# Kernel tuning notes

Measured on AMD Instinct MI355X. Metric: run time of the kernel, lower is better.

The kernel has to match this reference:

```python
import jax, jax.numpy as jnp
import numpy as np

BLOCK = 16  # NVFP4 block size (per-block FP8 scale over 16 FP4 values)
FP4_GRID = jnp.array([0.0, 0.5, 1.0, 1.5, 2.0, 3.0, 4.0, 6.0], dtype=jnp.float32)
FP4_MIDS = jnp.array([0.25, 0.75, 1.25, 1.75, 2.5, 3.5, 5.0], dtype=jnp.float32)


def _quantize_fp4(v):
    # round-to-nearest onto the signed E2M1 grid {0,.5,1,1.5,2,3,4,6}
    a = jnp.clip(jnp.abs(v), 0.0, 6.0)
    idx = jnp.searchsorted(FP4_MIDS, a)
    return jnp.sign(v) * FP4_GRID[idx]


def _block_quantize(x):
    # returns (fp4 values, per-16-block scales) such that x ~= q * scale_blocked
    M, K = x.shape
    B = K // BLOCK
    xb = x.reshape(M, B, BLOCK)
    s = jnp.max(jnp.abs(xb), axis=-1) / 6.0 + 1e-8  # [M, B]
    q = _quantize_fp4(xb / s[:, :, None]).reshape(M, K)
    return q, s


def setup_inputs() -> dict:
    key = jax.random.key(0)
    k1, k2, k3 = jax.random.split(key, 3)
    M, K, N = 8192, 4096, 4096
    bsz, q_len = 4, 2048

    x_raw = jax.random.normal(k1, (M, K), dtype=jnp.float32)
    w_raw = jax.random.normal(k2, (N, K), dtype=jnp.float32) * 0.02

    # global weight scale as in NVFP4_reorder_quantize_w: max(w)/(448*6)
    scale_w_global = jnp.max(w_raw) / (448.0 * 6.0)
    qw, scale_w = _block_quantize(w_raw / scale_w_global)

    # activation global scale (produced upstream by the activation quantizer)
    scale_x_global = jnp.max(x_raw) / (448.0 * 6.0)
    qx, scale_x = _block_quantize(x_raw / scale_x_global)

    bias = jax.random.normal(k3, (N,), dtype=jnp.float32) * 0.01

    return {
        "qx": qx,                      # [M, K] FP4-grid values
        "scale_x": scale_x,            # [M, K//16] block scales
        "scale": scale_x_global,       # scalar global activation scale
        "qw": qw,                      # [N, K] FP4-grid values
        "scale_w": scale_w,            # [N, K//16] block scales
        "scale_w_global": scale_w_global,
        "bias": bias,                  # [N]
        "bsz": bsz,
        "q_len": q_len,
    }


def reference(qx, scale_x, scale, qw, scale_w, scale_w_global, bias, bsz, q_len):
    # Dequant-scaled GEMM: y = (qx .* sx)(qw .* sw)^T * (scale * scale_w_global) + bias
    M, K = qx.shape
    N = qw.shape[0]
    B = K // BLOCK
    xd = (qx.reshape(M, B, BLOCK) * scale_x[:, :, None]).reshape(M, K)
    wd = (qw.reshape(N, B, BLOCK) * scale_w[:, :, None]).reshape(N, K)
    y = jnp.einsum("mk,nk->mn", xd, wd) * (scale * scale_w_global)
    y = y + bias
    return y.reshape(bsz, q_len, -1)
```

## Files before the change

### kernel.cpp

```cpp
#include <hip/hip_runtime.h>
#include <cstdint>

#define K_DIM 4096
#define ROWB 13
#define NU   (K_DIM / 32)

typedef __bf16 bf16x8 __attribute__((ext_vector_type(8)));
typedef float f32x4 __attribute__((ext_vector_type(4)));

__device__ inline unsigned short f2bf(float f) {
    union { float f; unsigned int u; } v; v.f = f;
    unsigned int u = v.u;
    return (unsigned short)((u + 0x7FFFu + ((u >> 16) & 1u)) >> 16);
}

__device__ __forceinline__ void gload16(const void* g, void* l) {
    __builtin_amdgcn_global_load_lds(
        (const __attribute__((address_space(1))) unsigned int*)g,
        (__attribute__((address_space(3))) unsigned int*)l,
        16, 0, 0);
}

__global__ __launch_bounds__(256) void dequant2_kernel(
        const float* __restrict__ qx, const float* __restrict__ sx,
        unsigned short* __restrict__ xd, long t8x,
        const float* __restrict__ qw, const float* __restrict__ sw,
        unsigned short* __restrict__ wd, long t8w) {
    long i = (long)blockIdx.x * blockDim.x + threadIdx.x;
    if (i >= t8x + t8w) return;
    const float* q; const float* s; unsigned short* o;
    if (i < t8x) { q = qx; s = sx; o = xd; }
    else         { q = qw; s = sw; o = wd; i -= t8x; }
    long e = i * 8;
    float sc = s[e >> 4];
    float4 v0 = *(const float4*)(q + e);
    float4 v1 = *(const float4*)(q + e + 4);
    union { unsigned short h[8]; uint4 u; } ov;
    ov.h[0] = f2bf(v0.x * sc); ov.h[1] = f2bf(v0.y * sc);
    ov.h[2] = f2bf(v0.z * sc); ov.h[3] = f2bf(v0.w * sc);
    ov.h[4] = f2bf(v1.x * sc); ov.h[5] = f2bf(v1.y * sc);
    ov.h[6] = f2bf(v1.z * sc); ov.h[7] = f2bf(v1.w * sc);
    *(uint4*)(o + e) = ov.u;
}


__global__ __launch_bounds__(256, 2) void gemm128x256_kernel(
        const unsigned short* __restrict__ A,
        const unsigned short* __restrict__ B,
        const float* __restrict__ sg1, const float* __restrict__ sg2,
        const float* __restrict__ bias,
        float* __restrict__ out, int M, int N) {
    __shared__ __align__(16) char lds[73728];

    const int tid  = threadIdx.x;
    const int lane = tid & 63;
    const int wid  = tid >> 6;
    const int l15  = lane & 15;
    const int cb   = (lane >> 4) << 4;
    const int scb  = ((lane & 3) ^ ((lane >> 3) & 3)) << 4;

    const int nbn = N >> 8;
    const int nwg = (M >> 7) * nbn;
    const int cpx = nwg >> 3;
    const int bid = blockIdx.x;
    const int swz = (bid & 7) * cpx + (bid >> 3);
    const int tile_m = (swz / nbn) << 7;
    const int tile_n = (swz % nbn) << 8;

    const int grow = lane >> 2;
    const char* gA0 = (const char*)A +
        ((size_t)(tile_m + 32 * wid + grow) << ROWB) + scb;
    const char* gB0 = (const char*)B +
        ((size_t)(tile_n + 64 * wid + grow) << ROWB) + scb;
    const int dA0 = wid * 2048;
    const int dB0 = 8192 + wid * 4096;

    const int aoff = l15 * 64 + (cb ^ (((l15 >> 1) & 3) << 4));
    const int brow = wid * 64 + l15;
    const int boff = 8192 + brow * 64 + (cb ^ (((brow >> 1) & 3) << 4));

    f32x4 acc[8][4];
#pragma unroll
    for (int mb = 0; mb < 8; ++mb)
#pragma unroll
        for (int nb = 0; nb < 4; ++nb) acc[mb][nb] = (f32x4){0.f, 0.f, 0.f, 0.f};

#pragma unroll
    for (int pu = 0; pu < 2; ++pu) {
        char* Sb = lds + pu * 24576;
        const int kb = pu << 6;
        gload16(gA0 + kb, Sb + dA0);
        gload16(gA0 + kb + ((size_t)16 << ROWB), Sb + dA0 + 1024);
        gload16(gB0 + kb, Sb + dB0);
        gload16(gB0 + kb + ((size_t)16 << ROWB), Sb + dB0 + 1024);
        gload16(gB0 + kb + ((size_t)32 << ROWB), Sb + dB0 + 2048);
        gload16(gB0 + kb + ((size_t)48 << ROWB), Sb + dB0 + 3072);
    }
    asm volatile("s_waitcnt vmcnt(6)" ::: "memory");
    __builtin_amdgcn_s_barrier();

#define UNIT_BODY(SKU, CUR, STG) do {                                        \
    const int skb = (SKU) << 6;                                              \
    bf16x8 bfr[4], afr[4], afr2[4];                                          \
    _Pragma("unroll")                                                        \
    for (int nb = 0; nb < 4; ++nb)                                           \
        bfr[nb] = *(const bf16x8*)(lds + (CUR) + boff + nb * 1024);          \
    _Pragma("unroll")                                                        \
    for (int mb = 0; mb < 4; ++mb)                                           \
        afr[mb] = *(const bf16x8*)(lds + (CUR) + aoff + mb * 1024);          \
    gload16(gA0 + skb, lds + (STG) + dA0);                                   \
    gload16(gA0 + skb + ((size_t)16 << ROWB), lds + (STG) + dA0 + 1024);     \
    gload16(gB0 + skb, lds + (STG) + dB0);                                   \
    __builtin_amdgcn_s_barrier();                                            \
    __builtin_amdgcn_s_setprio(1);                                           \
    _Pragma("unroll")                                                        \
    for (int mb = 0; mb < 4; ++mb)                                           \
        _Pragma("unroll")                                                    \
        for (int nb = 0; nb < 4; ++nb)                                       \
            acc[mb][nb] = __builtin_amdgcn_mfma_f32_16x16x32_bf16(           \
                afr[mb], bfr[nb], acc[mb][nb], 0, 0, 0);                     \
    __builtin_amdgcn_s_setprio(0);                                           \
    _Pragma("unroll")                                                        \
    for (int mb = 0; mb < 4; ++mb)                                           \
        afr2[mb] = *(const bf16x8*)(lds + (CUR) + aoff + 4096 + mb * 1024);  \
    gload16(gB0 + skb + ((size_t)16 << ROWB), lds + (STG) + dB0 + 1024);     \
    gload16(gB0 + skb + ((size_t)32 << ROWB), lds + (STG) + dB0 + 2048);     \
    gload16(gB0 + skb + ((size_t)48 << ROWB), lds + (STG) + dB0 + 3072);     \
    __builtin_amdgcn_s_barrier();                                            \
    __builtin_amdgcn_s_setprio(1);                                           \
    _Pragma("unroll")                                                        \
    for (int mb = 0; mb < 4; ++mb)                                           \
        _Pragma("unroll")                                                    \
        for (int nb = 0; nb < 4; ++nb)                                       \
            acc[mb + 4][nb] = __builtin_amdgcn_mfma_f32_16x16x32_bf16(       \
                afr2[mb], bfr[nb], acc[mb + 4][nb], 0, 0, 0);                \
    __builtin_amdgcn_s_setprio(0);                                           \
    asm volatile("s_waitcnt vmcnt(6)" ::: "memory");                         \
    __builtin_amdgcn_s_barrier();                                            \
} while (0)

    for (int ub = 0; ub < 126; ub += 3) {
        UNIT_BODY(ub + 2, 0,     49152);
        UNIT_BODY(ub + 3, 24576, 0);
        UNIT_BODY(ub + 4, 49152, 24576);
    }
    UNIT_BODY(127, 0,     49152);
    UNIT_BODY(127, 24576, 0);
#undef UNIT_BODY

    const float gs = sg1[0] * sg2[0];
    const int row0 = tile_m + ((lane >> 4) << 2);
    const int col0 = tile_n + wid * 64 + l15;
    float bv[4];
#pragma unroll
    for (int nb = 0; nb < 4; ++nb) bv[nb] = bias[col0 + nb * 16];
#pragma unroll
    for (int mb = 0; mb < 8; ++mb)
#pragma unroll
        for (int nb = 0; nb < 4; ++nb) {
            const int col = col0 + nb * 16;
#pragma unroll
            for (int j = 0; j < 4; ++j)
                out[(size_t)(row0 + mb * 16 + j) * N + col] =
                    acc[mb][nb][j] * gs + bv[nb];
        }
}

__global__ __launch_bounds__(256) void gemm_fused_kernel(
        const float* __restrict__ qx, const float* __restrict__ sx,
        const float* __restrict__ qw, const float* __restrict__ sw,
        const float* __restrict__ sg1, const float* __restrict__ sg2,
        const float* __restrict__ bias,
        float* __restrict__ out, int M, int N) {
    __shared__ __align__(16) unsigned short As[128 * 32];
    __shared__ __align__(16) unsigned short Bs[128 * 32];
    const int tid  = threadIdx.x;
    const int lane = tid & 63;
    const int wid  = tid >> 6;
    const int tile_n = blockIdx.x * 128;
    const int tile_m = blockIdx.y * 128;
    const int wm = wid >> 1, wn = wid & 1;
    f32x4 acc[16];
#pragma unroll
    for (int i = 0; i < 16; ++i) acc[i] = (f32x4){0.f, 0.f, 0.f, 0.f};
    const int l15 = lane & 15;
    const int lk  = (lane >> 4) * 8;
    for (int kt = 0; kt < K_DIM / 32; ++kt) {
#pragma unroll
        for (int cc = 0; cc < 2; ++cc) {
            const int c   = tid + cc * 256;
            const int row = c >> 2;
            const int col = (c & 3) * 8;
            const int gk  = kt * 32 + col;
            {
                const float* qp = qx + (long)(tile_m + row) * K_DIM + gk;
                float s = sx[(long)(tile_m + row) * (K_DIM / 16) + (gk >> 4)];
                float4 a0 = *(const float4*)qp;
                float4 a1 = *(const float4*)(qp + 4);
                union { unsigned short h[8]; uint4 u; } o;
                o.h[0] = f2bf(a0.x * s); o.h[1] = f2bf(a0.y * s);
                o.h[2] = f2bf(a0.z * s); o.h[3] = f2bf(a0.w * s);
                o.h[4] = f2bf(a1.x * s); o.h[5] = f2bf(a1.y * s);
                o.h[6] = f2bf(a1.z * s); o.h[7] = f2bf(a1.w * s);
                *(uint4*)&As[row * 32 + col] = o.u;
            }
            {
                const float* qp = qw + (long)(tile_n + row) * K_DIM + gk;
                float s = sw[(long)(tile_n + row) * (K_DIM / 16) + (gk >> 4)];
                float4 a0 = *(const float4*)qp;
                float4 a1 = *(const float4*)(qp + 4);
                union { unsigned short h[8]; uint4 u; } o;
                o.h[0] = f2bf(a0.x * s); o.h[1] = f2bf(a0.y * s);
                o.h[2] = f2bf(a0.z * s); o.h[3] = f2bf(a0.w * s);
                o.h[4] = f2bf(a1.x * s); o.h[5] = f2bf(a1.y * s);
                o.h[6] = f2bf(a1.z * s); o.h[7] = f2bf(a1.w * s);
                *(uint4*)&Bs[row * 32 + col] = o.u;
            }
        }
        __syncthreads();
        const unsigned short* pa = As + (wm * 64 + l15) * 32 + lk;
        const unsigned short* pb = Bs + (wn * 64 + l15) * 32 + lk;
        bf16x8 a[4], b[4];
#pragma unroll
        for (int i = 0; i < 4; ++i) {
            a[i] = *(const bf16x8*)(pa + i * 16 * 32);
            b[i] = *(const bf16x8*)(pb + i * 16 * 32);
        }
#pragma unroll
        for (int mi = 0; mi < 4; ++mi)
#pragma unroll
            for (int ni = 0; ni < 4; ++ni)
                acc[mi * 4 + ni] = __builtin_amdgcn_mfma_f32_16x16x32_bf16(
                    a[mi], b[ni], acc[mi * 4 + ni], 0, 0, 0);
        __syncthreads();
    }
    const float gs = sg1[0] * sg2[0];
    const int row0 = tile_m + wm * 64 + (lane >> 4) * 4;
    const int col0 = tile_n + wn * 64 + l15;
#pragma unroll
    for (int mi = 0; mi < 4; ++mi)
#pragma unroll
        for (int ni = 0; ni < 4; ++ni) {
            const int col = col0 + ni * 16;
            const float bv = bias[col];
#pragma unroll
            for (int j = 0; j < 4; ++j)
                out[(long)(row0 + mi * 16 + j) * N + col] =
                    acc[mi * 4 + ni][j] * gs + bv;
        }
}

extern "C" void kernel_launch(void* const* d_in, const int* in_sizes, int n_in,
                              void* d_out, int out_size, void* d_ws, size_t ws_size,
                              hipStream_t stream) {
    const float* qx   = (const float*)d_in[0];
    const float* sx   = (const float*)d_in[1];
    const float* sc   = (const float*)d_in[2];
    const float* qw   = (const float*)d_in[3];
    const float* sw   = (const float*)d_in[4];
    const float* swg  = (const float*)d_in[5];
    const float* bias = (const float*)d_in[6];
    float* out = (float*)d_out;

    const int M = in_sizes[0] / K_DIM;
    const int N = in_sizes[3] / K_DIM;

    const size_t needA = (size_t)M * K_DIM * sizeof(unsigned short);
    const size_t needB = (size_t)N * K_DIM * sizeof(unsigned short);

    if (ws_size >= needA + needB) {
        unsigned short* xd = (unsigned short*)d_ws;
        unsigned short* wd = (unsigned short*)((char*)d_ws + needA);
        long t8x = (long)M * K_DIM / 8;
        long t8w = (long)N * K_DIM / 8;
        long tot = t8x + t8w;
        dequant2_kernel<<<(int)((tot + 255) / 256), 256, 0, stream>>>(
            qx, sx, xd, t8x, qw, sw, wd, t8w);
        const int nwg = (M / 128) * (N / 256);
        gemm128x256_kernel<<<nwg, 256, 0, stream>>>(xd, wd, sc, swg, bias, out, M, N);
    } else {
        dim3 grid(N / 128, M / 128);
        gemm_fused_kernel<<<grid, 256, 0, stream>>>(
            qx, sx, qw, sw, sc, swg, bias, out, M, N);
    }
}
```

Baseline: 323.3 us.

## Use 256x256 tiles with 8 waves, streaming B fragments from global into registers

```diff
diff --git a/kernel.cpp b/kernel.cpp
--- a/kernel.cpp
+++ b/kernel.cpp
@@ -44,40 +44,42 @@
 }
 
 
-__global__ __launch_bounds__(256, 2) void gemm128x256_kernel(
+__global__ __launch_bounds__(512, 2) void gemm256_kernel(
         const unsigned short* __restrict__ A,
         const unsigned short* __restrict__ B,
         const float* __restrict__ sg1, const float* __restrict__ sg2,
         const float* __restrict__ bias,
         float* __restrict__ out, int M, int N) {
-    __shared__ __align__(16) char lds[73728];
+    __shared__ __align__(16) char lds[65536];
 
     const int tid  = threadIdx.x;
     const int lane = tid & 63;
     const int wid  = tid >> 6;
+    const int wm   = wid >> 2;
+    const int wn   = wid & 3;
     const int l15  = lane & 15;
     const int cb   = (lane >> 4) << 4;
     const int scb  = ((lane & 3) ^ ((lane >> 3) & 3)) << 4;
 
-    const int nbn = N >> 8;
-    const int nwg = (M >> 7) * nbn;
+    const int nbm = M >> 8;
+    const int nwg = nbm * (N >> 8);
     const int cpx = nwg >> 3;
     const int bid = blockIdx.x;
     const int swz = (bid & 7) * cpx + (bid >> 3);
-    const int tile_m = (swz / nbn) << 7;
-    const int tile_n = (swz % nbn) << 8;
+    const int tile_n = (swz / nbm) << 8;
+    const int tile_m = (swz % nbm) << 8;
 
     const int grow = lane >> 2;
     const char* gA0 = (const char*)A +
         ((size_t)(tile_m + 32 * wid + grow) << ROWB) + scb;
-    const char* gB0 = (const char*)B +
-        ((size_t)(tile_n + 64 * wid + grow) << ROWB) + scb;
+    const char* gA1 = gA0 + ((size_t)16 << ROWB);
     const int dA0 = wid * 2048;
-    const int dB0 = 8192 + wid * 4096;
-
-    const int aoff = l15 * 64 + (cb ^ (((l15 >> 1) & 3) << 4));
-    const int brow = wid * 64 + l15;
-    const int boff = 8192 + brow * 64 + (cb ^ (((brow >> 1) & 3) << 4));
+
+    const int arow = wm * 128 + l15;
+    const int aoff = arow * 64 + (cb ^ (((arow >> 1) & 3) << 4));
+
+    const char* gBf = (const char*)B +
+        ((size_t)(tile_n + wn * 64 + l15) << ROWB) + cb;
 
     f32x4 acc[8][4];
 #pragma unroll
@@ -85,72 +87,56 @@
 #pragma unroll
         for (int nb = 0; nb < 4; ++nb) acc[mb][nb] = (f32x4){0.f, 0.f, 0.f, 0.f};
 
+    bf16x8 bAr[4], bBr[4];
+
+#pragma unroll
+    for (int nb = 0; nb < 4; ++nb)
+        bAr[nb] = *(const bf16x8*)(gBf + ((size_t)nb << 17));
 #pragma unroll
     for (int pu = 0; pu < 2; ++pu) {
-        char* Sb = lds + pu * 24576;
+        char* Sb = lds + pu * 16384;
         const int kb = pu << 6;
         gload16(gA0 + kb, Sb + dA0);
-        gload16(gA0 + kb + ((size_t)16 << ROWB), Sb + dA0 + 1024);
-        gload16(gB0 + kb, Sb + dB0);
-        gload16(gB0 + kb + ((size_t)16 << ROWB), Sb + dB0 + 1024);
-        gload16(gB0 + kb + ((size_t)32 << ROWB), Sb + dB0 + 2048);
-        gload16(gB0 + kb + ((size_t)48 << ROWB), Sb + dB0 + 3072);
-    }
-    asm volatile("s_waitcnt vmcnt(6)" ::: "memory");
+        gload16(gA1 + kb, Sb + dA0 + 1024);
+    }
+    asm volatile("s_waitcnt vmcnt(2)" ::: "memory");
     __builtin_amdgcn_s_barrier();
 
-#define UNIT_BODY(SKU, CUR, STG) do {                                        \
-    const int skb = (SKU) << 6;                                              \
-    bf16x8 bfr[4], afr[4], afr2[4];                                          \
+#define UNIT_BODY(U, CUR, STG, BCUR, BNXT) do {                              \
+    const int un = ((U) + 1 < NU) ? (U) + 1 : (NU - 1);                      \
+    const int us = ((U) + 2 < NU) ? (U) + 2 : (NU - 1);                      \
     _Pragma("unroll")                                                        \
     for (int nb = 0; nb < 4; ++nb)                                           \
-        bfr[nb] = *(const bf16x8*)(lds + (CUR) + boff + nb * 1024);          \
+        BNXT[nb] = *(const bf16x8*)(gBf + ((size_t)nb << 17) + un * 64);     \
+    gload16(gA0 + (us << 6), lds + (STG) + dA0);                             \
+    gload16(gA1 + (us << 6), lds + (STG) + dA0 + 1024);                      \
+    bf16x8 afr[8];                                                           \
     _Pragma("unroll")                                                        \
-    for (int mb = 0; mb < 4; ++mb)                                           \
+    for (int mb = 0; mb < 8; ++mb)                                           \
         afr[mb] = *(const bf16x8*)(lds + (CUR) + aoff + mb * 1024);          \
-    gload16(gA0 + skb, lds + (STG) + dA0);                                   \
-    gload16(gA0 + skb + ((size_t)16 << ROWB), lds + (STG) + dA0 + 1024);     \
-    gload16(gB0 + skb, lds + (STG) + dB0);                                   \
-    __builtin_amdgcn_s_barrier();                                            \
     __builtin_amdgcn_s_setprio(1);                                           \
     _Pragma("unroll")                                                        \
-    for (int mb = 0; mb < 4; ++mb)                                           \
+    for (int mb = 0; mb < 8; ++mb)                                           \
         _Pragma("unroll")                                                    \
         for (int nb = 0; nb < 4; ++nb)                                       \
             acc[mb][nb] = __builtin_amdgcn_mfma_f32_16x16x32_bf16(           \
-                afr[mb], bfr[nb], acc[mb][nb], 0, 0, 0);                     \
+                afr[mb], BCUR[nb], acc[mb][nb], 0, 0, 0);                    \
     __builtin_amdgcn_s_setprio(0);                                           \
-    _Pragma("unroll")                                                        \
-    for (int mb = 0; mb < 4; ++mb)                                           \
-        afr2[mb] = *(const bf16x8*)(lds + (CUR) + aoff + 4096 + mb * 1024);  \
-    gload16(gB0 + skb + ((size_t)16 << ROWB), lds + (STG) + dB0 + 1024);     \
-    gload16(gB0 + skb + ((size_t)32 << ROWB), lds + (STG) + dB0 + 2048);     \
-    gload16(gB0 + skb + ((size_t)48 << ROWB), lds + (STG) + dB0 + 3072);     \
-    __builtin_amdgcn_s_barrier();                                            \
-    __builtin_amdgcn_s_setprio(1);                                           \
-    _Pragma("unroll")                                                        \
-    for (int mb = 0; mb < 4; ++mb)                                           \
-        _Pragma("unroll")                                                    \
-        for (int nb = 0; nb < 4; ++nb)                                       \
-            acc[mb + 4][nb] = __builtin_amdgcn_mfma_f32_16x16x32_bf16(       \
-                afr2[mb], bfr[nb], acc[mb + 4][nb], 0, 0, 0);                \
-    __builtin_amdgcn_s_setprio(0);                                           \
-    asm volatile("s_waitcnt vmcnt(6)" ::: "memory");                         \
+    asm volatile("s_waitcnt vmcnt(2)" ::: "memory");                         \
     __builtin_amdgcn_s_barrier();                                            \
 } while (0)
 
-    for (int ub = 0; ub < 126; ub += 3) {
-        UNIT_BODY(ub + 2, 0,     49152);
-        UNIT_BODY(ub + 3, 24576, 0);
-        UNIT_BODY(ub + 4, 49152, 24576);
-    }
-    UNIT_BODY(127, 0,     49152);
-    UNIT_BODY(127, 24576, 0);
+    for (int ub = 0; ub < NU; ub += 4) {
+        UNIT_BODY(ub + 0, 0,     32768, bAr, bBr);
+        UNIT_BODY(ub + 1, 16384, 49152, bBr, bAr);
+        UNIT_BODY(ub + 2, 32768, 0,     bAr, bBr);
+        UNIT_BODY(ub + 3, 49152, 16384, bBr, bAr);
+    }
 #undef UNIT_BODY
 
     const float gs = sg1[0] * sg2[0];
-    const int row0 = tile_m + ((lane >> 4) << 2);
-    const int col0 = tile_n + wid * 64 + l15;
+    const int row0 = tile_m + wm * 128 + ((lane >> 4) << 2);
+    const int col0 = tile_n + wn * 64 + l15;
     float bv[4];
 #pragma unroll
     for (int nb = 0; nb < 4; ++nb) bv[nb] = bias[col0 + nb * 16];
@@ -276,8 +262,8 @@
         long tot = t8x + t8w;
         dequant2_kernel<<<(int)((tot + 255) / 256), 256, 0, stream>>>(
             qx, sx, xd, t8x, qw, sw, wd, t8w);
-        const int nwg = (M / 128) * (N / 256);
-        gemm128x256_kernel<<<nwg, 256, 0, stream>>>(xd, wd, sc, swg, bias, out, M, N);
+        const int nwg = (M / 256) * (N / 256);
+        gemm256_kernel<<<nwg, 512, 0, stream>>>(xd, wd, sc, swg, bias, out, M, N);
     } else {
         dim3 grid(N / 128, M / 128);
         gemm_fused_kernel<<<grid, 256, 0, stream>>>(
```

Result: slower. 442.2 us (+36.8%).
